# Kernel tuning notes

Hardware: AMD Instinct MI355X
Metric: run time of the kernel (lower is better)

## Reference

```python
import jax, jax.numpy as jnp
import numpy as np

M, K, D = 8, 4096, 512  # groups, codes per group, total dim
DG = D // M             # per-group dim = 64


def setup_inputs() -> dict:
    key = jax.random.key(0)
    k1, k2, k3 = jax.random.split(key, 3)
    codes = jax.random.randint(k1, (32, 64, 64, M), 0, K, dtype=jnp.int32)
    codebook = jax.random.normal(k2, (M, K, DG), dtype=jnp.float32)
    wv = jax.random.normal(k3, (M, DG, DG), dtype=jnp.float32) / np.sqrt(DG)
    return {"codes": codes, "codebook": codebook, "wv": wv}


def reference(codes, codebook, wv):
    # v[m,k,c] = sum_d codebook[m,k,d] * wv[m,c,d]  (small per-group GEMM)
    v = jnp.einsum('mkd,mcd->mkc', codebook, wv)  # [M, K, DG]
    # one-hot matmul over k is exactly an indexed gather:
    # gathered[n,h,w,m,c] = v[m, codes[n,h,w,m], c]
    m_idx = jnp.arange(v.shape[0])  # [M]
    gathered = v[m_idx[None, None, None, :], codes]  # [n,h,w,M,DG]
    n, h, w = codes.shape[:3]
    out = gathered.reshape(n, h, w, -1)          # [n,h,w,D]
    return jnp.transpose(out, (0, 3, 1, 2))      # [n,D,h,w]
```

## Files before the change

### kernel.cpp

```cpp
#include <hip/hip_runtime.h>
#include <hip/hip_bf16.h>

#define MQ 8
#define KQ 4096
#define DG 64
#define NN 32
#define HW 4096
#define DD 512
#define THW 128

__global__ __launch_bounds__(256) void compute_v_kernel(
    const float* __restrict__ codebook,
    const float* __restrict__ wv,
    float* __restrict__ v) {
  __shared__ float wv_t[DG][DG + 1];
  __shared__ float cb[64][DG];

  const int m = blockIdx.y;
  const int k0 = blockIdx.x * 64;
  const int tid = threadIdx.x;

  const float4* wvm4 = (const float4*)(wv + (size_t)m * DG * DG);
  for (int i = tid; i < DG * DG / 4; i += 256) {
    int c = i >> 4, d4 = (i & 15) * 4;
    float4 val = wvm4[i];
    wv_t[d4 + 0][c] = val.x;
    wv_t[d4 + 1][c] = val.y;
    wv_t[d4 + 2][c] = val.z;
    wv_t[d4 + 3][c] = val.w;
  }
  const float4* cbm4 = (const float4*)(codebook + ((size_t)m * KQ + k0) * DG);
  float4* cb4 = (float4*)&cb[0][0];
  for (int i = tid; i < 64 * DG / 4; i += 256) cb4[i] = cbm4[i];
  __syncthreads();

  const int c = tid & 63;
  const int kq = tid >> 6;

  float acc[16];
#pragma unroll
  for (int kl = 0; kl < 16; ++kl) acc[kl] = 0.f;

  for (int d4 = 0; d4 < DG; d4 += 4) {
    float w0 = wv_t[d4 + 0][c];
    float w1 = wv_t[d4 + 1][c];
    float w2 = wv_t[d4 + 2][c];
    float w3 = wv_t[d4 + 3][c];
#pragma unroll
    for (int kl = 0; kl < 16; ++kl) {
      float4 cbv = *(const float4*)&cb[kq * 16 + kl][d4];
      acc[kl] += cbv.x * w0 + cbv.y * w1 + cbv.z * w2 + cbv.w * w3;
    }
  }

  float* vout = v + ((size_t)m * KQ + k0) * DG;
#pragma unroll
  for (int kl = 0; kl < 16; ++kl) {
    vout[(size_t)(kq * 16 + kl) * DG + c] = acc[kl];
  }
}

__global__ __launch_bounds__(256) void gather_kernel(
    const int* __restrict__ codes,
    const float* __restrict__ v,
    float* __restrict__ out) {
  __shared__ int scode[THW];
  __shared__ float tile[THW][DG + 1];

  const int b = blockIdx.x;
  const int m = b & 7;
  const int t = b >> 3;
  const int n = t & 31;
  const int tileidx = t >> 5;
  const int hw0 = tileidx * THW;

  const int tid = threadIdx.x;
  const int w = tid >> 6;
  const int l = tid & 63;

  if (tid < THW) {
    scode[tid] = codes[((size_t)n * HW + hw0 + tid) * MQ + m];
  }
  __syncthreads();

  const float* vm = v + (size_t)m * KQ * DG;
#pragma unroll 8
  for (int jj = 0; jj < 32; ++jj) {
    int j = w * 32 + jj;
    int r = scode[j];
    tile[j][l] = vm[(size_t)r * DG + l];
  }
  __syncthreads();

  float* outb = out + ((size_t)n * DD + (size_t)m * DG) * HW + hw0;
#pragma unroll 4
  for (int u = 0; u < 16; ++u) {
    int up = w * 16 + u;
    int c = up >> 1;
    int half = up & 1;
    int j = half * 64 + l;
    float val0 = tile[j][c];
    float val1 = tile[j][c + 32];
    __builtin_nontemporal_store(val0, outb + (size_t)c * HW + j);
    __builtin_nontemporal_store(val1, outb + (size_t)(c + 32) * HW + j);
  }
}

extern "C" void kernel_launch(void* const* d_in, const int* in_sizes, int n_in,
                              void* d_out, int out_size, void* d_ws, size_t ws_size,
                              hipStream_t stream) {
  const int* codes = (const int*)d_in[0];
  const float* codebook = (const float*)d_in[1];
  const float* wv = (const float*)d_in[2];
  float* out = (float*)d_out;
  float* v = (float*)d_ws;

  compute_v_kernel<<<dim3(64, 8), 256, 0, stream>>>(codebook, wv, v);
  gather_kernel<<<NN * MQ * (HW / THW), 256, 0, stream>>>(codes, v, out);
}
```

Measured before the change: 316.8 us.

## Widen gather tile to 256 positions and stage channels in two halves with float4 loads

The gather kernel now processes 256 spatial positions per block instead of 128, so each block does more work and the grid is half as large. To keep shared memory small, the 64 channels are staged in two 32-channel halves through a 256x33 tile, with an extra barrier per half. Codebook rows are read with float4 loads instead of scalar loads to cut the number of load instructions. The trade-off is more synchronisation per block and fewer blocks for latency hiding.

```diff
diff --git a/kernel.cpp b/kernel.cpp
--- a/kernel.cpp
+++ b/kernel.cpp
@@ -7,7 +7,8 @@
 #define NN 32
 #define HW 4096
 #define DD 512
-#define THW 128
+#define THW 256
+#define TS 33
 
 __global__ __launch_bounds__(256) void compute_v_kernel(
     const float* __restrict__ codebook,
@@ -65,44 +66,52 @@
     const float* __restrict__ v,
     float* __restrict__ out) {
   __shared__ int scode[THW];
-  __shared__ float tile[THW][DG + 1];
+  __shared__ float tile[THW][TS];
 
   const int b = blockIdx.x;
   const int m = b & 7;
   const int t = b >> 3;
   const int n = t & 31;
-  const int tileidx = t >> 5;
-  const int hw0 = tileidx * THW;
+  const int hw0 = (t >> 5) * THW;
 
   const int tid = threadIdx.x;
   const int w = tid >> 6;
   const int l = tid & 63;
 
-  if (tid < THW) {
-    scode[tid] = codes[((size_t)n * HW + hw0 + tid) * MQ + m];
-  }
+  scode[tid] = codes[((size_t)n * HW + hw0 + tid) * MQ + m];
   __syncthreads();
 
   const float* vm = v + (size_t)m * KQ * DG;
-#pragma unroll 8
-  for (int jj = 0; jj < 32; ++jj) {
-    int j = w * 32 + jj;
-    int r = scode[j];
-    tile[j][l] = vm[(size_t)r * DG + l];
-  }
-  __syncthreads();
+  float* outb = out + ((size_t)n * DD + (size_t)m * DG) * HW + hw0;
 
-  float* outb = out + ((size_t)n * DD + (size_t)m * DG) * HW + hw0;
-#pragma unroll 4
-  for (int u = 0; u < 16; ++u) {
-    int up = w * 16 + u;
-    int c = up >> 1;
-    int half = up & 1;
-    int j = half * 64 + l;
-    float val0 = tile[j][c];
-    float val1 = tile[j][c + 32];
-    __builtin_nontemporal_store(val0, outb + (size_t)c * HW + j);
-    __builtin_nontemporal_store(val1, outb + (size_t)(c + 32) * HW + j);
+#pragma unroll
+  for (int ch = 0; ch < 2; ++ch) {
+#pragma unroll
+    for (int iter = 0; iter < 8; ++iter) {
+      int i = iter * 256 + tid;
+      int j = i >> 3;
+      int bq = i & 7;
+      int r = scode[j];
+      float4 val = *(const float4*)(vm + (size_t)r * DG + ch * 32 + bq * 4);
+      tile[j][bq * 4 + 0] = val.x;
+      tile[j][bq * 4 + 1] = val.y;
+      tile[j][bq * 4 + 2] = val.z;
+      tile[j][bq * 4 + 3] = val.w;
+    }
+    __syncthreads();
+
+#pragma unroll
+    for (int u = 0; u < 8; ++u) {
+      int cc = w * 8 + u;
+      int c = ch * 32 + cc;
+#pragma unroll
+      for (int q = 0; q < 4; ++q) {
+        int j = q * 64 + l;
+        __builtin_nontemporal_store(tile[j][cc],
+                                    outb + (size_t)c * HW + j);
+      }
+    }
+    __syncthreads();
   }
 }
 
```

Result: faster. 301.7 us (-4.8%).
